# Optimization experiments

Hardware: AMD Instinct MI355X
Metric: run time of the kernel (lower is better)

Reference implementation:

```python
import jax, jax.numpy as jnp
import numpy as np

N_USERS = 16384
EMB_DIM = 32
N_EDGES = 524288  # N_USERS * avg_degree 32


def setup_inputs() -> dict:
    key = jax.random.key(0)
    k1, k2, k3, k4, k5 = jax.random.split(key, 5)
    social_emb = jax.random.normal(k1, (N_USERS, EMB_DIM), dtype=jnp.float32)
    preference_emb = jax.random.normal(k2, (N_USERS, EMB_DIM), dtype=jnp.float32)
    # Jaccard similarities lie in [0, 1]
    attention_scores = jax.random.uniform(k3, (N_USERS, N_USERS), dtype=jnp.float32)
    uu_graph = jax.random.randint(k4, (2, N_EDGES), 0, N_USERS, dtype=jnp.int64)
    return {
        "social_emb": social_emb,
        "preference_emb": preference_emb,
        "attention_scores": attention_scores,
        "uu_graph": uu_graph,
    }


def reference(social_emb, preference_emb, attention_scores, uu_graph):
    # The original per-user Python loop:
    #   final[i] = sum_j attention_scores[i, j] * preference_emb[j]
    # is exactly one dense [N,N] @ [N,D] matmul.
    final = attention_scores @ preference_emb  # [N, D]
    # prop_uu: one round of message passing over the user-user graph
    # (sum of source-user embeddings into each destination user).
    src, dst = uu_graph[0], uu_graph[1]
    out = jax.ops.segment_sum(final[src], dst, num_segments=final.shape[0])  # [N, D]
    # dropout is identity at inference (rate treated as 0)
    return out
```

## Files before the change

kernel.cpp:

```cpp
#include <hip/hip_runtime.h>
#include <hip/hip_bf16.h>

#define NUSERS 16384
#define DIM 32
#define NEDGES 524288
#define KCHUNK 32
#define NCHUNKS 512
#define KSPLIT 8
#define CPS (NCHUNKS / KSPLIT)
#define RPB 64
#define CAP 192

using f32x4  = __attribute__((ext_vector_type(4))) float;
using bf16x8 = __attribute__((ext_vector_type(8))) short;
using int4v  = __attribute__((ext_vector_type(4))) int;
using int2v  = __attribute__((ext_vector_type(2))) int;

static __device__ __forceinline__ short f2bf(float f) {
    __hip_bfloat16 h = __float2bfloat16(f);
    return __builtin_bit_cast(short, h);
}

static __device__ __forceinline__ bool detect_is64(const int* __restrict__ g) {
    bool is64 = true;
#pragma unroll
    for (int s = 0; s < 8; ++s) is64 &= (g[2 * s + 1] == 0);
    return is64;
}

__global__ void __launch_bounds__(256) prep_and_bucket(const float* __restrict__ P,
                                                       short* __restrict__ Pfrag,
                                                       const int* __restrict__ g,
                                                       int* __restrict__ cursor,
                                                       int* __restrict__ bucket) {
    if (blockIdx.x < 256) {
        int t = blockIdx.x * blockDim.x + threadIdx.x;
        int lane = t & 63;
        int h    = (t >> 6) & 1;
        int c    = t >> 7;
        int d    = h * 16 + (lane & 15);
        int gq   = lane >> 4;
        short tmp[8];
#pragma unroll
        for (int i = 0; i < 8; ++i)
            tmp[i] = f2bf(P[(size_t)(c * KCHUNK + gq * 8 + i) * DIM + d]);
        *reinterpret_cast<bf16x8*>(Pfrag + (size_t)t * 8) =
            *reinterpret_cast<bf16x8*>(tmp);
    } else {
        bool is64 = detect_is64(g);
        int e = (blockIdx.x - 256) * blockDim.x + threadIdx.x;
        int src, dst;
        if (is64) {
            const int2v* g2 = reinterpret_cast<const int2v*>(g);
            src = g2[e].x;
            dst = g2[NEDGES + e].x;
        } else {
            src = g[e];
            dst = g[NEDGES + e];
        }
        int p = atomicAdd(&cursor[dst], 1);
        if (p < CAP) bucket[(size_t)dst * CAP + p] = src;
    }
}

__global__ void __launch_bounds__(256) gemm_kernel(const float* __restrict__ A,
                                                   const short* __restrict__ Pfrag,
                                                   float* __restrict__ parts) {
    const int lane = threadIdx.x & 63;
    const int wave = threadIdx.x >> 6;
    const int r    = lane & 15;
    const int g    = lane >> 4;

    const int rowblk = blockIdx.x;
    const int kseg   = blockIdx.y;
    const int row    = rowblk * RPB + wave * 16 + r;
    const size_t arow = (size_t)row * NUSERS;

    f32x4 acc0 = {0.f, 0.f, 0.f, 0.f};
    f32x4 acc1 = {0.f, 0.f, 0.f, 0.f};

    const int c0 = kseg * CPS;
    for (int c = c0; c < c0 + CPS; ++c) {
        const float* ap = A + arow + (size_t)c * KCHUNK + g * 8;
        f32x4 a0 = *reinterpret_cast<const f32x4*>(ap);
        f32x4 a1 = *reinterpret_cast<const f32x4*>(ap + 4);
        bf16x8 af;
        af[0] = f2bf(a0[0]); af[1] = f2bf(a0[1]);
        af[2] = f2bf(a0[2]); af[3] = f2bf(a0[3]);
        af[4] = f2bf(a1[0]); af[5] = f2bf(a1[1]);
        af[6] = f2bf(a1[2]); af[7] = f2bf(a1[3]);

        const short* pf = Pfrag + (size_t)c * 1024;
        bf16x8 b0 = *reinterpret_cast<const bf16x8*>(pf + lane * 8);
        bf16x8 b1 = *reinterpret_cast<const bf16x8*>(pf + 512 + lane * 8);

        acc0 = __builtin_amdgcn_mfma_f32_16x16x32_bf16(af, b0, acc0, 0, 0, 0);
        acc1 = __builtin_amdgcn_mfma_f32_16x16x32_bf16(af, b1, acc1, 0, 0, 0);
    }

    float* part = parts + (size_t)kseg * NUSERS * DIM;
    const int out_row0 = rowblk * RPB + wave * 16 + g * 4;
#pragma unroll
    for (int q = 0; q < 4; ++q) {
        float* dst = part + (size_t)(out_row0 + q) * DIM + r;
        dst[0]  = acc0[q];
        dst[16] = acc1[q];
    }
}

__global__ void __launch_bounds__(256) reduce_partials(const float* __restrict__ parts,
                                                       float* __restrict__ fin) {
    int i = blockIdx.x * blockDim.x + threadIdx.x;
    const f32x4* p4 = reinterpret_cast<const f32x4*>(parts);
    f32x4 s = {0.f, 0.f, 0.f, 0.f};
#pragma unroll
    for (int k = 0; k < KSPLIT; ++k)
        s += p4[(size_t)k * (NUSERS * DIM / 4) + i];
    reinterpret_cast<f32x4*>(fin)[i] = s;
}

__global__ void __launch_bounds__(256) gather_kernel(const int* __restrict__ bucket,
                                                     const int* __restrict__ cursor,
                                                     const float* __restrict__ fin,
                                                     float* __restrict__ out) {
    int t = blockIdx.x * blockDim.x + threadIdx.x;
    int d = t >> 3;
    int q = t & 7;
    if (d >= NUSERS) return;
    int cnt = cursor[d];
    if (cnt > CAP) cnt = CAP;
    const int* bk = bucket + (size_t)d * CAP;
    const f32x4* f4 = reinterpret_cast<const f32x4*>(fin);
    f32x4 s = {0.f, 0.f, 0.f, 0.f};
    int i = 0;
    for (; i + 4 <= cnt; i += 4) {
        int4v s4 = *reinterpret_cast<const int4v*>(bk + i);
        s += f4[(size_t)s4.x * 8 + q];
        s += f4[(size_t)s4.y * 8 + q];
        s += f4[(size_t)s4.z * 8 + q];
        s += f4[(size_t)s4.w * 8 + q];
    }
    for (; i < cnt; ++i)
        s += f4[(size_t)bk[i] * 8 + q];
    reinterpret_cast<f32x4*>(out)[(size_t)d * 8 + q] = s;
}

extern "C" void kernel_launch(void* const* d_in, const int* in_sizes, int n_in,
                              void* d_out, int out_size, void* d_ws, size_t ws_size,
                              hipStream_t stream) {
    const float* pref = (const float*)d_in[1];
    const float* att  = (const float*)d_in[2];
    const int*   grph = (const int*)d_in[3];
    float* out = (float*)d_out;

    char* ws = (char*)d_ws;
    float* parts  = (float*)ws;
    float* fin    = (float*)(ws + (size_t)16 * 1024 * 1024);
    short* pfrag  = (short*)(ws + (size_t)18 * 1024 * 1024);
    int*   cursor = (int*)  (ws + (size_t)19 * 1024 * 1024);
    int*   bucket = (int*)  (ws + (size_t)20 * 1024 * 1024);

    hipMemsetAsync(cursor, 0, NUSERS * sizeof(int), stream);

    prep_and_bucket<<<dim3(256 + NEDGES / 256), dim3(256), 0, stream>>>(
        pref, pfrag, grph, cursor, bucket);

    gemm_kernel<<<dim3(NUSERS / RPB, KSPLIT), dim3(256), 0, stream>>>(att, pfrag, parts);

    reduce_partials<<<dim3(NUSERS * DIM / 4 / 256), dim3(256), 0, stream>>>(parts, fin);

    gather_kernel<<<dim3(NUSERS * 8 / 256), dim3(256), 0, stream>>>(bucket, cursor, fin, out);
}
```

Baseline: 256.3 us.

## Overlap edge bucketing with GEMM, fold memset into prep, split gather per destination

After: 261.8 us. 1.02x slower.

```diff
diff --git a/kernel.cpp b/kernel.cpp
--- a/kernel.cpp
+++ b/kernel.cpp
@@ -10,10 +10,10 @@
 #define CPS (NCHUNKS / KSPLIT)
 #define RPB 64
 #define CAP 192
+#define NBBUCKET 256
 
 using f32x4  = __attribute__((ext_vector_type(4))) float;
 using bf16x8 = __attribute__((ext_vector_type(8))) short;
-using int4v  = __attribute__((ext_vector_type(4))) int;
 using int2v  = __attribute__((ext_vector_type(2))) int;
 
 static __device__ __forceinline__ short f2bf(float f) {
@@ -28,51 +28,59 @@
     return is64;
 }
 
-__global__ void __launch_bounds__(256) prep_and_bucket(const float* __restrict__ P,
-                                                       short* __restrict__ Pfrag,
-                                                       const int* __restrict__ g,
-                                                       int* __restrict__ cursor,
-                                                       int* __restrict__ bucket) {
-    if (blockIdx.x < 256) {
-        int t = blockIdx.x * blockDim.x + threadIdx.x;
-        int lane = t & 63;
-        int h    = (t >> 6) & 1;
-        int c    = t >> 7;
-        int d    = h * 16 + (lane & 15);
-        int gq   = lane >> 4;
-        short tmp[8];
+__global__ void __launch_bounds__(256) prep_pfrag(const float* __restrict__ P,
+                                                  short* __restrict__ Pfrag,
+                                                  int* __restrict__ cursor) {
+    int t = blockIdx.x * blockDim.x + threadIdx.x;
+    if (t < NUSERS) cursor[t] = 0;
+    int lane = t & 63;
+    int h    = (t >> 6) & 1;
+    int c    = t >> 7;
+    int d    = h * 16 + (lane & 15);
+    int gq   = lane >> 4;
+    short tmp[8];
 #pragma unroll
-        for (int i = 0; i < 8; ++i)
-            tmp[i] = f2bf(P[(size_t)(c * KCHUNK + gq * 8 + i) * DIM + d]);
-        *reinterpret_cast<bf16x8*>(Pfrag + (size_t)t * 8) =
-            *reinterpret_cast<bf16x8*>(tmp);
-    } else {
-        bool is64 = detect_is64(g);
-        int e = (blockIdx.x - 256) * blockDim.x + threadIdx.x;
-        int src, dst;
-        if (is64) {
-            const int2v* g2 = reinterpret_cast<const int2v*>(g);
-            src = g2[e].x;
-            dst = g2[NEDGES + e].x;
-        } else {
-            src = g[e];
-            dst = g[NEDGES + e];
-        }
-        int p = atomicAdd(&cursor[dst], 1);
-        if (p < CAP) bucket[(size_t)dst * CAP + p] = src;
-    }
+    for (int i = 0; i < 8; ++i)
+        tmp[i] = f2bf(P[(size_t)(c * KCHUNK + gq * 8 + i) * DIM + d]);
+    *reinterpret_cast<bf16x8*>(Pfrag + (size_t)t * 8) =
+        *reinterpret_cast<bf16x8*>(tmp);
 }
 
-__global__ void __launch_bounds__(256) gemm_kernel(const float* __restrict__ A,
+__global__ void __launch_bounds__(256) gemm_bucket(const float* __restrict__ A,
                                                    const short* __restrict__ Pfrag,
-                                                   float* __restrict__ parts) {
+                                                   float* __restrict__ parts,
+                                                   const int* __restrict__ g,
+                                                   int* __restrict__ cursor,
+                                                   int* __restrict__ bucket) {
+    if (blockIdx.x < NBBUCKET) {
+        bool is64 = detect_is64(g);
+        int base = blockIdx.x * (NEDGES / NBBUCKET);
+#pragma unroll
+        for (int k = 0; k < NEDGES / NBBUCKET / 256; ++k) {
+            int e = base + k * 256 + threadIdx.x;
+            int src, dst;
+            if (is64) {
+                const int2v* g2 = reinterpret_cast<const int2v*>(g);
+                src = g2[e].x;
+                dst = g2[NEDGES + e].x;
+            } else {
+                src = g[e];
+                dst = g[NEDGES + e];
+            }
+            int p = atomicAdd(&cursor[dst], 1);
+            if (p < CAP) bucket[(size_t)dst * CAP + p] = src;
+        }
+        return;
+    }
+
+    const int gb   = blockIdx.x - NBBUCKET;
     const int lane = threadIdx.x & 63;
     const int wave = threadIdx.x >> 6;
     const int r    = lane & 15;
-    const int g    = lane >> 4;
+    const int gq   = lane >> 4;
 
-    const int rowblk = blockIdx.x;
-    const int kseg   = blockIdx.y;
+    const int rowblk = gb & 255;
+    const int kseg   = gb >> 8;
     const int row    = rowblk * RPB + wave * 16 + r;
     const size_t arow = (size_t)row * NUSERS;
 
@@ -80,8 +88,9 @@
     f32x4 acc1 = {0.f, 0.f, 0.f, 0.f};
 
     const int c0 = kseg * CPS;
+#pragma unroll 2
     for (int c = c0; c < c0 + CPS; ++c) {
-        const float* ap = A + arow + (size_t)c * KCHUNK + g * 8;
+        const float* ap = A + arow + (size_t)c * KCHUNK + gq * 8;
         f32x4 a0 = *reinterpret_cast<const f32x4*>(ap);
         f32x4 a1 = *reinterpret_cast<const f32x4*>(ap + 4);
         bf16x8 af;
@@ -99,7 +108,7 @@
     }
 
     float* part = parts + (size_t)kseg * NUSERS * DIM;
-    const int out_row0 = rowblk * RPB + wave * 16 + g * 4;
+    const int out_row0 = rowblk * RPB + wave * 16 + gq * 4;
 #pragma unroll
     for (int q = 0; q < 4; ++q) {
         float* dst = part + (size_t)(out_row0 + q) * DIM + r;
@@ -124,25 +133,31 @@
                                                      const float* __restrict__ fin,
                                                      float* __restrict__ out) {
     int t = blockIdx.x * blockDim.x + threadIdx.x;
-    int d = t >> 3;
-    int q = t & 7;
+    int d = t >> 4;
+    int q = (t >> 1) & 7;
+    int h = t & 1;
     if (d >= NUSERS) return;
     int cnt = cursor[d];
     if (cnt > CAP) cnt = CAP;
+    int beg = h ? (cnt >> 1) : 0;
+    int end = h ? cnt : (cnt >> 1);
     const int* bk = bucket + (size_t)d * CAP;
     const f32x4* f4 = reinterpret_cast<const f32x4*>(fin);
-    f32x4 s = {0.f, 0.f, 0.f, 0.f};
-    int i = 0;
-    for (; i + 4 <= cnt; i += 4) {
-        int4v s4 = *reinterpret_cast<const int4v*>(bk + i);
-        s += f4[(size_t)s4.x * 8 + q];
-        s += f4[(size_t)s4.y * 8 + q];
-        s += f4[(size_t)s4.z * 8 + q];
-        s += f4[(size_t)s4.w * 8 + q];
+    f32x4 s0 = {0.f, 0.f, 0.f, 0.f};
+    f32x4 s1 = {0.f, 0.f, 0.f, 0.f};
+    int i = beg;
+    for (; i + 2 <= end; i += 2) {
+        s0 += f4[(size_t)bk[i]     * 8 + q];
+        s1 += f4[(size_t)bk[i + 1] * 8 + q];
     }
-    for (; i < cnt; ++i)
-        s += f4[(size_t)bk[i] * 8 + q];
-    reinterpret_cast<f32x4*>(out)[(size_t)d * 8 + q] = s;
+    if (i < end) s0 += f4[(size_t)bk[i] * 8 + q];
+    f32x4 s = s0 + s1;
+    s.x += __shfl_xor(s.x, 1);
+    s.y += __shfl_xor(s.y, 1);
+    s.z += __shfl_xor(s.z, 1);
+    s.w += __shfl_xor(s.w, 1);
+    if (h == 0)
+        reinterpret_cast<f32x4*>(out)[(size_t)d * 8 + q] = s;
 }
 
 extern "C" void kernel_launch(void* const* d_in, const int* in_sizes, int n_in,
@@ -160,14 +175,12 @@
     int*   cursor = (int*)  (ws + (size_t)19 * 1024 * 1024);
     int*   bucket = (int*)  (ws + (size_t)20 * 1024 * 1024);
 
-    hipMemsetAsync(cursor, 0, NUSERS * sizeof(int), stream);
+    prep_pfrag<<<dim3(256), dim3(256), 0, stream>>>(pref, pfrag, cursor);
 
-    prep_and_bucket<<<dim3(256 + NEDGES / 256), dim3(256), 0, stream>>>(
-        pref, pfrag, grph, cursor, bucket);
-
-    gemm_kernel<<<dim3(NUSERS / RPB, KSPLIT), dim3(256), 0, stream>>>(att, pfrag, parts);
+    gemm_bucket<<<dim3(NBBUCKET + (NUSERS / RPB) * KSPLIT), dim3(256), 0, stream>>>(
+        att, pfrag, parts, grph, cursor, bucket);
 
     reduce_partials<<<dim3(NUSERS * DIM / 4 / 256), dim3(256), 0, stream>>>(parts, fin);
 
-    gather_kernel<<<dim3(NUSERS * 8 / 256), dim3(256), 0, stream>>>(bucket, cursor, fin, out);
+    gather_kernel<<<dim3(NUSERS * 16 / 256), dim3(256), 0, stream>>>(bucket, cursor, fin, out);
 }
```

## Stage A tiles through per-wave swizzled LDS with register prefetch double-buffering

Applied to the files above, without the earlier changes.

Measured after the change: 249.3 us. -2.7%, faster.

```diff
diff --git a/kernel.cpp b/kernel.cpp
--- a/kernel.cpp
+++ b/kernel.cpp
@@ -8,11 +8,14 @@
 #define NCHUNKS 512
 #define KSPLIT 8
 #define CPS (NCHUNKS / KSPLIT)
+#define KTILE 128
+#define NTILES (CPS * KCHUNK / KTILE)
 #define RPB 64
 #define CAP 192
 
 using f32x4  = __attribute__((ext_vector_type(4))) float;
 using bf16x8 = __attribute__((ext_vector_type(8))) short;
+using s16x4  = __attribute__((ext_vector_type(4))) short;
 using int4v  = __attribute__((ext_vector_type(4))) int;
 using int2v  = __attribute__((ext_vector_type(2))) int;
 
@@ -63,43 +66,75 @@
     }
 }
 
-__global__ void __launch_bounds__(256) gemm_kernel(const float* __restrict__ A,
-                                                   const short* __restrict__ Pfrag,
-                                                   float* __restrict__ parts) {
+__global__ void __launch_bounds__(256, 4) gemm_kernel(const float* __restrict__ A,
+                                                      const short* __restrict__ Pfrag,
+                                                      float* __restrict__ parts) {
+    __shared__ short lds[4][2][16][128];
+
     const int lane = threadIdx.x & 63;
     const int wave = threadIdx.x >> 6;
     const int r    = lane & 15;
-    const int g    = lane >> 4;
+    const int gq   = lane >> 4;
 
     const int rowblk = blockIdx.x;
     const int kseg   = blockIdx.y;
-    const int row    = rowblk * RPB + wave * 16 + r;
-    const size_t arow = (size_t)row * NUSERS;
+    const int row0   = rowblk * RPB + wave * 16;
+    const int c0     = kseg * CPS;
+
+    const int srow  = lane >> 5;
+    const int scolf = (lane & 31) * 4;
+    const float* Abase = A + (size_t)row0 * NUSERS + (size_t)c0 * KCHUNK;
+
+    short* myl = &lds[wave][0][0][0];
 
     f32x4 acc0 = {0.f, 0.f, 0.f, 0.f};
     f32x4 acc1 = {0.f, 0.f, 0.f, 0.f};
-
-    const int c0 = kseg * CPS;
-    for (int c = c0; c < c0 + CPS; ++c) {
-        const float* ap = A + arow + (size_t)c * KCHUNK + g * 8;
-        f32x4 a0 = *reinterpret_cast<const f32x4*>(ap);
-        f32x4 a1 = *reinterpret_cast<const f32x4*>(ap + 4);
-        bf16x8 af;
-        af[0] = f2bf(a0[0]); af[1] = f2bf(a0[1]);
-        af[2] = f2bf(a0[2]); af[3] = f2bf(a0[3]);
-        af[4] = f2bf(a1[0]); af[5] = f2bf(a1[1]);
-        af[6] = f2bf(a1[2]); af[7] = f2bf(a1[3]);
-
-        const short* pf = Pfrag + (size_t)c * 1024;
-        bf16x8 b0 = *reinterpret_cast<const bf16x8*>(pf + lane * 8);
-        bf16x8 b1 = *reinterpret_cast<const bf16x8*>(pf + 512 + lane * 8);
-
-        acc0 = __builtin_amdgcn_mfma_f32_16x16x32_bf16(af, b0, acc0, 0, 0, 0);
-        acc1 = __builtin_amdgcn_mfma_f32_16x16x32_bf16(af, b1, acc1, 0, 0, 0);
+    f32x4 sreg[8];
+
+    auto issue = [&](int t) {
+#pragma unroll
+        for (int k = 0; k < 8; ++k)
+            sreg[k] = *reinterpret_cast<const f32x4*>(
+                Abase + (size_t)(2 * k + srow) * NUSERS + t * KTILE + scolf);
+    };
+    auto commit = [&](int t) {
+        short* buf = myl + (t & 1) * (16 * 128);
+#pragma unroll
+        for (int k = 0; k < 8; ++k) {
+            int rl = 2 * k + srow;
+            int cb = ((lane & 31) * 8) ^ ((rl & 7) << 4);
+            s16x4 v = {f2bf(sreg[k][0]), f2bf(sreg[k][1]),
+                       f2bf(sreg[k][2]), f2bf(sreg[k][3])};
+            *reinterpret_cast<s16x4*>(buf + rl * 128 + (cb >> 1)) = v;
+        }
+        asm volatile("s_waitcnt lgkmcnt(0)" ::: "memory");
+        __builtin_amdgcn_sched_barrier(0);
+    };
+    auto compute = [&](int t) {
+        const short* buf = myl + (t & 1) * (16 * 128);
+#pragma unroll
+        for (int cc = 0; cc < 4; ++cc) {
+            int c = c0 + t * 4 + cc;
+            const short* pf = Pfrag + (size_t)c * 1024;
+            bf16x8 b0 = *reinterpret_cast<const bf16x8*>(pf + lane * 8);
+            bf16x8 b1 = *reinterpret_cast<const bf16x8*>(pf + 512 + lane * 8);
+            int cb = (cc * 64 + gq * 16) ^ ((r & 7) << 4);
+            bf16x8 af = *reinterpret_cast<const bf16x8*>(buf + r * 128 + (cb >> 1));
+            acc0 = __builtin_amdgcn_mfma_f32_16x16x32_bf16(af, b0, acc0, 0, 0, 0);
+            acc1 = __builtin_amdgcn_mfma_f32_16x16x32_bf16(af, b1, acc1, 0, 0, 0);
+        }
+    };
+
+    issue(0);
+    commit(0);
+    for (int t = 0; t < NTILES; ++t) {
+        if (t + 1 < NTILES) issue(t + 1);
+        compute(t);
+        if (t + 1 < NTILES) commit(t + 1);
     }
 
     float* part = parts + (size_t)kseg * NUSERS * DIM;
-    const int out_row0 = rowblk * RPB + wave * 16 + g * 4;
+    const int out_row0 = rowblk * RPB + wave * 16 + gq * 4;
 #pragma unroll
     for (int q = 0; q < 4; ++q) {
         float* dst = part + (size_t)(out_row0 + q) * DIM + r;
```

## Replace split-K GEMM with register/LDS double-buffered full-K kernel

Applied to the files above, without the earlier changes.

Result: faster. 218.7 us (-14.7%).

```diff
diff --git a/kernel.cpp b/kernel.cpp
--- a/kernel.cpp
+++ b/kernel.cpp
@@ -5,14 +5,14 @@
 #define DIM 32
 #define NEDGES 524288
 #define KCHUNK 32
-#define NCHUNKS 512
-#define KSPLIT 8
-#define CPS (NCHUNKS / KSPLIT)
+#define KTILE 256
+#define NTILES (NUSERS / KTILE)
 #define RPB 64
 #define CAP 192
 
 using f32x4  = __attribute__((ext_vector_type(4))) float;
 using bf16x8 = __attribute__((ext_vector_type(8))) short;
+using s16x4  = __attribute__((ext_vector_type(4))) short;
 using int4v  = __attribute__((ext_vector_type(4))) int;
 using int2v  = __attribute__((ext_vector_type(2))) int;
 
@@ -63,60 +63,86 @@
     }
 }
 
-__global__ void __launch_bounds__(256) gemm_kernel(const float* __restrict__ A,
-                                                   const short* __restrict__ Pfrag,
-                                                   float* __restrict__ parts) {
+__global__ void __launch_bounds__(256, 1) gemm_kernel(const float* __restrict__ A,
+                                                      const short* __restrict__ Pfrag,
+                                                      float* __restrict__ fin) {
+    __shared__ short lds[4][2][16][256];
+
     const int lane = threadIdx.x & 63;
     const int wave = threadIdx.x >> 6;
     const int r    = lane & 15;
-    const int g    = lane >> 4;
+    const int gq   = lane >> 4;
 
-    const int rowblk = blockIdx.x;
-    const int kseg   = blockIdx.y;
-    const int row    = rowblk * RPB + wave * 16 + r;
-    const size_t arow = (size_t)row * NUSERS;
+    const int row0 = blockIdx.x * RPB + wave * 16;
+    const float* Abase = A + (size_t)row0 * NUSERS;
 
-    f32x4 acc0 = {0.f, 0.f, 0.f, 0.f};
-    f32x4 acc1 = {0.f, 0.f, 0.f, 0.f};
+    short* buf0 = &lds[wave][0][0][0];
+    short* buf1 = &lds[wave][1][0][0];
 
-    const int c0 = kseg * CPS;
-    for (int c = c0; c < c0 + CPS; ++c) {
-        const float* ap = A + arow + (size_t)c * KCHUNK + g * 8;
-        f32x4 a0 = *reinterpret_cast<const f32x4*>(ap);
-        f32x4 a1 = *reinterpret_cast<const f32x4*>(ap + 4);
-        bf16x8 af;
-        af[0] = f2bf(a0[0]); af[1] = f2bf(a0[1]);
-        af[2] = f2bf(a0[2]); af[3] = f2bf(a0[3]);
-        af[4] = f2bf(a1[0]); af[5] = f2bf(a1[1]);
-        af[6] = f2bf(a1[2]); af[7] = f2bf(a1[3]);
+    f32x4  acc0 = {0.f, 0.f, 0.f, 0.f};
+    f32x4  acc1 = {0.f, 0.f, 0.f, 0.f};
+    f32x4  sreg[16];
+    bf16x8 bregA[16], bregB[16];
 
-        const short* pf = Pfrag + (size_t)c * 1024;
-        bf16x8 b0 = *reinterpret_cast<const bf16x8*>(pf + lane * 8);
-        bf16x8 b1 = *reinterpret_cast<const bf16x8*>(pf + 512 + lane * 8);
+    auto issueA = [&](int t) {
+#pragma unroll
+        for (int k = 0; k < 16; ++k)
+            sreg[k] = *reinterpret_cast<const f32x4*>(
+                Abase + (size_t)k * NUSERS + t * KTILE + lane * 4);
+    };
+    auto issueB = [&](int t, bf16x8* br) {
+        const short* pf = Pfrag + (size_t)t * 8192;
+#pragma unroll
+        for (int cc = 0; cc < 8; ++cc) {
+            br[2 * cc]     = *reinterpret_cast<const bf16x8*>(pf + cc * 1024 + lane * 8);
+            br[2 * cc + 1] = *reinterpret_cast<const bf16x8*>(pf + cc * 1024 + 512 + lane * 8);
+        }
+    };
+    auto commitT = [&](short* buf) {
+#pragma unroll
+        for (int k = 0; k < 16; ++k) {
+            int cb = (lane * 8) ^ ((k & 7) << 4);
+            s16x4 v = {f2bf(sreg[k][0]), f2bf(sreg[k][1]),
+                       f2bf(sreg[k][2]), f2bf(sreg[k][3])};
+            *reinterpret_cast<s16x4*>(buf + k * 256 + (cb >> 1)) = v;
+        }
+        asm volatile("s_waitcnt lgkmcnt(0)" ::: "memory");
+        __builtin_amdgcn_sched_barrier(0);
+    };
+    auto computeT = [&](const bf16x8* br, const short* buf) {
+#pragma unroll
+        for (int cc = 0; cc < 8; ++cc) {
+            int cb = (cc * 64 + gq * 16) ^ ((r & 7) << 4);
+            bf16x8 af = *reinterpret_cast<const bf16x8*>(buf + r * 256 + (cb >> 1));
+            acc0 = __builtin_amdgcn_mfma_f32_16x16x32_bf16(af, br[2 * cc],     acc0, 0, 0, 0);
+            acc1 = __builtin_amdgcn_mfma_f32_16x16x32_bf16(af, br[2 * cc + 1], acc1, 0, 0, 0);
+        }
+    };
 
-        acc0 = __builtin_amdgcn_mfma_f32_16x16x32_bf16(af, b0, acc0, 0, 0, 0);
-        acc1 = __builtin_amdgcn_mfma_f32_16x16x32_bf16(af, b1, acc1, 0, 0, 0);
+    issueB(0, bregA);
+    issueA(0);
+    commitT(buf0);
+
+    for (int t = 0; t < NTILES; t += 2) {
+        issueB(t + 1, bregB);
+        issueA(t + 1);
+        computeT(bregA, buf0);
+        commitT(buf1);
+        if (t + 2 < NTILES) {
+            issueB(t + 2, bregA);
+            issueA(t + 2);
+        }
+        computeT(bregB, buf1);
+        if (t + 2 < NTILES) commitT(buf0);
     }
 
-    float* part = parts + (size_t)kseg * NUSERS * DIM;
-    const int out_row0 = rowblk * RPB + wave * 16 + g * 4;
+    const int out_row0 = row0 + gq * 4;
 #pragma unroll
     for (int q = 0; q < 4; ++q) {
-        float* dst = part + (size_t)(out_row0 + q) * DIM + r;
+        float* dst = fin + (size_t)(out_row0 + q) * DIM + r;
         dst[0]  = acc0[q];
         dst[16] = acc1[q];
     }
-}
-
-__global__ void __launch_bounds__(256) reduce_partials(const float* __restrict__ parts,
-                                                       float* __restrict__ fin) {
-    int i = blockIdx.x * blockDim.x + threadIdx.x;
-    const f32x4* p4 = reinterpret_cast<const f32x4*>(parts);
-    f32x4 s = {0.f, 0.f, 0.f, 0.f};
-#pragma unroll
-    for (int k = 0; k < KSPLIT; ++k)
-        s += p4[(size_t)k * (NUSERS * DIM / 4) + i];
-    reinterpret_cast<f32x4*>(fin)[i] = s;
 }
 
 __global__ void __launch_bounds__(256) gather_kernel(const int* __restrict__ bucket,
@@ -154,8 +180,7 @@
     float* out = (float*)d_out;
 
     char* ws = (char*)d_ws;
-    float* parts  = (float*)ws;
-    float* fin    = (float*)(ws + (size_t)16 * 1024 * 1024);
+    float* fin    = (float*)ws;
     short* pfrag  = (short*)(ws + (size_t)18 * 1024 * 1024);
     int*   cursor = (int*)  (ws + (size_t)19 * 1024 * 1024);
     int*   bucket = (int*)  (ws + (size_t)20 * 1024 * 1024);
@@ -165,9 +190,7 @@
     prep_and_bucket<<<dim3(256 + NEDGES / 256), dim3(256), 0, stream>>>(
         pref, pfrag, grph, cursor, bucket);
 
-    gemm_kernel<<<dim3(NUSERS / RPB, KSPLIT), dim3(256), 0, stream>>>(att, pfrag, parts);
-
-    reduce_partials<<<dim3(NUSERS * DIM / 4 / 256), dim3(256), 0, stream>>>(parts, fin);
+    gemm_kernel<<<dim3(NUSERS / RPB), dim3(256), 0, stream>>>(att, pfrag, fin);
 
     gather_kernel<<<dim3(NUSERS * 8 / 256), dim3(256), 0, stream>>>(bucket, cursor, fin, out);
 }
```
